# Performance work log

Measured on AMD Instinct MI355X. Metric: run time of the kernel, lower is better.

The kernel has to match this reference:

```python
import jax, jax.numpy as jnp
import numpy as np

B, C, P, NP = 16, 768, 2048, 64
FFE = 4


def _ln(x, g, b, eps=1e-5):
    m = jnp.mean(x, axis=-1, keepdims=True)
    v = jnp.mean(jnp.square(x - m), axis=-1, keepdims=True)
    return (x - m) * jax.lax.rsqrt(v + eps) * g + b


def _gelu(x):
    return jax.nn.gelu(x, approximate=False)  # torch nn.GELU default (erf)


def _any_attn(q, k, v, nqg, nqb, nkg, nkb, nvg, nvb, wq, wk, wv, wp, bq, bk, bv, bp):
    # AnyAttention: LN each stream, project, ReLU-gated logits scaled by d^-0.5, softmax, proj
    scale = q.shape[-1] ** -0.5
    qn = _ln(q, nqg, nqb) @ wq + bq
    kn = _ln(k, nkg, nkb) @ wk + bk
    vn = _ln(v, nvg, nvb) @ wv + bv
    attn = jnp.einsum('bqc,bkc->bqk', qn, kn)
    attn = jax.nn.relu(attn) * scale  # returned attn is relu*scale (pre-softmax)
    out = jnp.einsum('bqk,bkc->bqc', jax.nn.softmax(attn, axis=-1), vn)
    return attn, out @ wp + bp


def _forward(x, parts,
             enc_nq_g, enc_nq_b, enc_nk_g, enc_nk_b, enc_nv_g, enc_nv_b,
             enc_wq, enc_wk, enc_wv, enc_wp, enc_bq, enc_bk, enc_bv, enc_bp,
             dec_nq_g, dec_nq_b, dec_nk_g, dec_nk_b, dec_nv_g, dec_nv_b,
             dec_wq, dec_wk, dec_wv, dec_wp, dec_bq, dec_bk, dec_bv, dec_bp,
             ffn_ng, ffn_nb, ffn_w1, ffn_b1, ffn_w2, ffn_b2,
             sr_w1, sr_b1, sr_w2, sr_b2):
    x = jnp.swapaxes(x, 1, 2)  # b c p -> b p c
    # SimpleReasoning: SE-style gate over part tokens (AdaptiveMaxPool1d(1) = max over channel dim)
    g = jnp.max(parts, axis=-1)                                  # [b, np]
    g = _gelu(g @ sr_w1 + sr_b1)
    gate = jax.nn.sigmoid(g @ sr_w2 + sr_b2)[..., None]          # [b, np, 1]
    parts = gate * parts + parts                                 # parts1 + parts (residual)
    # enc_attn: parts attend over image tokens
    attn0, attn_out = _any_attn(parts, x, x,
                                enc_nq_g, enc_nq_b, enc_nk_g, enc_nk_b, enc_nv_g, enc_nv_b,
                                enc_wq, enc_wk, enc_wv, enc_wp, enc_bq, enc_bk, enc_bv, enc_bp)
    attn_0 = jnp.max(attn0, axis=-1)                             # maxpool over k -> [b, np]
    parts_in = parts + attn_out
    # FFN on image tokens with residual
    h = _ln(x, ffn_ng, ffn_nb)
    feats1 = x + (_gelu(h @ ffn_w1 + ffn_b1) @ ffn_w2 + ffn_b2)
    # dec_attn: image tokens attend over part tokens
    _, feats = _any_attn(feats1, parts_in, parts_in,
                         dec_nq_g, dec_nq_b, dec_nk_g, dec_nk_b, dec_nv_g, dec_nv_b,
                         dec_wq, dec_wk, dec_wv, dec_wp, dec_bq, dec_bk, dec_bv, dec_bp)
    feats = x + feats
    return jnp.swapaxes(feats, 1, 2), attn_0                     # [b, c, p], [b, np]


def setup_inputs() -> dict:
    key = jax.random.key(0)
    ki = iter(jax.random.split(key, 48))
    def rn(shape, s=1.0):
        return jax.random.normal(next(ki), shape, jnp.float32) * s
    d = {}
    d['x'] = rn((B, C, P))
    d['parts'] = rn((B, NP, C))
    for pre in ('enc', 'dec'):
        for nm in ('nq', 'nk', 'nv'):
            d[f'{pre}_{nm}_g'] = jnp.ones((C,), jnp.float32)
            d[f'{pre}_{nm}_b'] = jnp.zeros((C,), jnp.float32)
        for nm in ('wq', 'wk', 'wv', 'wp'):
            d[f'{pre}_{nm}'] = rn((C, C), 0.02)
        for nm in ('bq', 'bk', 'bv', 'bp'):
            d[f'{pre}_{nm}'] = jnp.zeros((C,), jnp.float32)
    d['ffn_ng'] = jnp.ones((C,), jnp.float32)
    d['ffn_nb'] = jnp.zeros((C,), jnp.float32)
    d['ffn_w1'] = rn((C, FFE * C), 0.02)
    d['ffn_b1'] = jnp.zeros((FFE * C,), jnp.float32)
    d['ffn_w2'] = rn((FFE * C, C), 0.02)
    d['ffn_b2'] = jnp.zeros((C,), jnp.float32)
    d['sr_w1'] = rn((NP, NP), 0.1)
    d['sr_b1'] = jnp.zeros((NP,), jnp.float32)
    d['sr_w2'] = rn((NP, NP), 0.1)
    d['sr_b2'] = jnp.zeros((NP,), jnp.float32)
    return d


def reference(x, parts,
              enc_nq_g, enc_nq_b, enc_nk_g, enc_nk_b, enc_nv_g, enc_nv_b,
              enc_wq, enc_wk, enc_wv, enc_wp, enc_bq, enc_bk, enc_bv, enc_bp,
              dec_nq_g, dec_nq_b, dec_nk_g, dec_nk_b, dec_nv_g, dec_nv_b,
              dec_wq, dec_wk, dec_wv, dec_wp, dec_bq, dec_bk, dec_bv, dec_bp,
              ffn_ng, ffn_nb, ffn_w1, ffn_b1, ffn_w2, ffn_b2,
              sr_w1, sr_b1, sr_w2, sr_b2):
    return _forward(x, parts,
                    enc_nq_g, enc_nq_b, enc_nk_g, enc_nk_b, enc_nv_g, enc_nv_b,
                    enc_wq, enc_wk, enc_wv, enc_wp, enc_bq, enc_bk, enc_bv, enc_bp,
                    dec_nq_g, dec_nq_b, dec_nk_g, dec_nk_b, dec_nv_g, dec_nv_b,
                    dec_wq, dec_wk, dec_wv, dec_wp, dec_bq, dec_bk, dec_bv, dec_bp,
                    ffn_ng, ffn_nb, ffn_w1, ffn_b1, ffn_w2, ffn_b2,
                    sr_w1, sr_b1, sr_w2, sr_b2)
```

## Files before the change

### kernel.cpp

```cpp
#include <hip/hip_runtime.h>

typedef unsigned short u16;
typedef unsigned int u32;
typedef __bf16 bf16x8 __attribute__((ext_vector_type(8)));
typedef float f32x4 __attribute__((ext_vector_type(4)));
typedef unsigned int u32x4 __attribute__((ext_vector_type(4)));

#define BB 16
#define CC 768
#define PP 2048
#define FF 3072

__device__ __forceinline__ float b2f(u16 u) {
  unsigned int x = ((unsigned int)u) << 16;
  return __builtin_bit_cast(float, x);
}
__device__ __forceinline__ u16 f2b(float f) {
  unsigned int x = __builtin_bit_cast(unsigned int, f);
  x += 0x7fffu + ((x >> 16) & 1u);
  return (u16)(x >> 16);
}
__device__ __forceinline__ float erf_fast(float x) {
  float ax = fabsf(x);
  float t = 1.0f / fmaf(0.3275911f, ax, 1.0f);
  float p = t * fmaf(t, fmaf(t, fmaf(t, fmaf(t, 1.061405429f, -1.453152027f),
                                     1.421413741f), -0.284496736f), 0.254829592f);
  float r = 1.0f - p * __expf(-ax * ax);
  return copysignf(r, x);
}
__device__ __forceinline__ float gelu_f(float x) {
  return 0.5f * x * (1.0f + erf_fast(x * 0.7071067811865475f));
}

typedef __attribute__((address_space(1))) const unsigned int g_u32;
typedef __attribute__((address_space(3))) unsigned int l_u32;
__device__ __forceinline__ void gl_lds16(const u16* g, u16* l) {
  __builtin_amdgcn_global_load_lds((g_u32*)g, (l_u32*)l, 16, 0, 0);
}

struct Wtr10 {
  const float* W[10]; const float* g[10]; u16* O[10];
  int Kd[10]; int Nd[10]; int tr[10]; int cum[11];
};
__global__ void wtr10_k(Wtr10 a) {
  __shared__ float t[64][65];
  int tbid = blockIdx.x;
  int z = 0;
  while (tbid >= a.cum[z + 1]) ++z;
  int r = tbid - a.cum[z];
  const float* W = a.W[z];
  const float* g = a.g[z];
  u16* Wt = a.O[z];
  int K = a.Kd[z], N = a.Nd[z];
  int nbx = N >> 6;
  int n0 = (r % nbx) * 64, k0 = (r / nbx) * 64;
  int tx = threadIdx.x & 63, ty = threadIdx.x >> 6;
  if (!a.tr[z]) {
    for (int i = 0; i < 16; ++i) {
      int k = k0 + ty + i * 4;
      float sc = g ? g[k] : 1.0f;
      Wt[(long)k * N + n0 + tx] = f2b(W[(long)k * N + n0 + tx] * sc);
    }
    return;
  }
  for (int i = 0; i < 16; ++i) {
    int k = k0 + ty + i * 4;
    float sc = g ? g[k] : 1.0f;
    t[ty + i * 4][tx] = W[(long)k * N + n0 + tx] * sc;
  }
  __syncthreads();
  for (int i = 0; i < 16; ++i) {
    int n = n0 + ty + i * 4;
    Wt[(long)n * K + k0 + tx] = f2b(t[tx][ty + i * 4]);
  }
}

struct Bf7 {
  const float* b[7]; const float* nb[7]; const float* W[7]; float* o[7];
  int Kd[7]; int Nd[7];
};
__global__ void bfuse7_k(Bf7 a) {
  __shared__ float red[4][64];
  int tbid = blockIdx.x;
  int z, bx;
  if (tbid < 72) { z = tbid / 12; bx = tbid % 12; }
  else { z = 6; bx = tbid - 72; }
  const float* b = a.b[z];
  const float* nb = a.nb[z];
  const float* W = a.W[z];
  float* outb = a.o[z];
  int K = a.Kd[z], N = a.Nd[z];
  int n = bx * 64 + (threadIdx.x & 63);
  int slice = threadIdx.x >> 6;
  float acc = 0.f;
#pragma unroll 4
  for (int k = slice; k < K; k += 4) acc += nb[k] * W[(long)k * N + n];
  red[slice][threadIdx.x & 63] = acc;
  __syncthreads();
  if (slice == 0)
    outb[n] = b[n] + red[0][threadIdx.x & 63] + red[1][threadIdx.x & 63] +
              red[2][threadIdx.x & 63] + red[3][threadIdx.x & 63];
}

__global__ void bfuse1_k(const float* __restrict__ b, const float* __restrict__ nb,
                         const float* __restrict__ W, float* __restrict__ outb) {
  __shared__ float red[4][64];
  int n = blockIdx.x * 64 + (threadIdx.x & 63);
  int slice = threadIdx.x >> 6;
  float acc = 0.f;
#pragma unroll 4
  for (int k = slice; k < CC; k += 4) acc += nb[k] * W[(long)k * CC + n];
  red[slice][threadIdx.x & 63] = acc;
  __syncthreads();
  if (slice == 0)
    outb[n] = b[n] + red[0][threadIdx.x & 63] + red[1][threadIdx.x & 63] +
              red[2][threadIdx.x & 63] + red[3][threadIdx.x & 63];
}

__global__ void dot_k(const u16* __restrict__ A, int stride,
                      const float* __restrict__ vec, float* __restrict__ outp) {
  int row = blockIdx.x * 4 + (threadIdx.x >> 6);
  int lane = threadIdx.x & 63;
  const u16* ip = A + (long)row * stride;
  float s = 0.f;
  for (int i = 0; i < 12; ++i) s += b2f(ip[lane + i * 64]) * vec[lane + i * 64];
  for (int o = 32; o; o >>= 1) s += __shfl_xor(s, o);
  if (lane == 0) outp[row] = s;
}

__global__ void xprep_k(const float* __restrict__ x, float* __restrict__ mean,
                        float* __restrict__ rstd, u16* __restrict__ xh) {
  __shared__ float t[64][65];
  __shared__ float red[8][64];
  __shared__ float mn_s[64], rs_s[64];
  int p0 = blockIdx.x * 64, b = blockIdx.y;
  int tx = threadIdx.x & 63, ty = threadIdx.x >> 6;
  const float* xb = x + (long)b * CC * PP;
  float s = 0.f, sq = 0.f;
  for (int c = ty; c < CC; c += 4) {
    float f = xb[(long)c * PP + p0 + tx];
    s += f; sq += f * f;
  }
  red[ty][tx] = s;
  red[4 + ty][tx] = sq;
  __syncthreads();
  if (ty == 0) {
    float S = red[0][tx] + red[1][tx] + red[2][tx] + red[3][tx];
    float Q = red[4][tx] + red[5][tx] + red[6][tx] + red[7][tx];
    float m = S * (1.0f / 768.0f);
    float var = Q * (1.0f / 768.0f) - m * m;
    float rs = rsqrtf(var + 1e-5f);
    mn_s[tx] = m; rs_s[tx] = rs;
    int gi = (b << 11) + p0 + tx;
    mean[gi] = m; rstd[gi] = rs;
  }
  __syncthreads();
  u16* ob = xh + (long)b * PP * CC;
  for (int cb = 0; cb < 12; ++cb) {
    int c0 = cb * 64;
    for (int i = 0; i < 16; ++i)
      t[ty + i * 4][tx] = xb[(long)(c0 + ty + i * 4) * PP + p0 + tx];
    __syncthreads();
    for (int i = 0; i < 16; ++i) {
      int pl = ty + i * 4;
      ob[(long)(p0 + pl) * CC + c0 + tx] = f2b((t[tx][pl] - mn_s[pl]) * rs_s[pl]);
    }
    __syncthreads();
  }
}

__global__ void parts_gate_k(const float* __restrict__ parts,
                             const float* __restrict__ w1, const float* __restrict__ b1,
                             const float* __restrict__ w2, const float* __restrict__ b2,
                             float* __restrict__ gate_out) {
  int b = blockIdx.x, t = threadIdx.x;
  __shared__ float g[64], g1[64];
  int r = t >> 2, l4 = t & 3;
  const float* pr = parts + ((long)b * 64 + r) * CC;
  float m = -1e30f;
  for (int c = l4; c < CC; c += 4) m = fmaxf(m, pr[c]);
  m = fmaxf(m, __shfl_xor(m, 1));
  m = fmaxf(m, __shfl_xor(m, 2));
  if (l4 == 0) g[r] = m;
  __syncthreads();
  if (t < 64) {
    float a = b1[t];
    for (int k = 0; k < 64; ++k) a += g[k] * w1[k * 64 + t];
    g1[t] = gelu_f(a);
  }
  __syncthreads();
  if (t < 64) {
    float a = b2[t];
    for (int k = 0; k < 64; ++k) a += g1[k] * w2[k * 64 + t];
    gate_out[b * 64 + t] = 1.0f / (1.0f + expf(-a));
  }
}

__global__ void gate_ln_k(const float* __restrict__ parts, const float* __restrict__ gate,
                          float* __restrict__ parts1, u16* __restrict__ ph) {
  int row = blockIdx.x * 4 + (threadIdx.x >> 6);
  int lane = threadIdx.x & 63;
  float g = 1.0f + gate[row];
  const float* ip = parts + (long)row * CC;
  float* op1 = parts1 + (long)row * CC;
  float v[12];
  float s = 0.f, sq = 0.f;
  for (int i = 0; i < 12; ++i) {
    float f = ip[lane + i * 64] * g;
    v[i] = f; op1[lane + i * 64] = f;
    s += f; sq += f * f;
  }
  for (int o = 32; o; o >>= 1) { s += __shfl_xor(s, o); sq += __shfl_xor(sq, o); }
  float mean = s * (1.0f / 768.0f);
  float var = sq * (1.0f / 768.0f) - mean * mean;
  float rstd = rsqrtf(var + 1e-5f);
  u16* op = ph + (long)row * CC;
  for (int i = 0; i < 12; ++i) op[lane + i * 64] = f2b((v[i] - mean) * rstd);
}

template <typename T>
__global__ void ln_rows_k(const T* __restrict__ in, u16* __restrict__ outp, int rows) {
  int row = blockIdx.x * 4 + (threadIdx.x >> 6);
  if (row >= rows) return;
  int lane = threadIdx.x & 63;
  const T* ip = in + (long)row * CC;
  float v[12];
  float s = 0.f, sq = 0.f;
  for (int i = 0; i < 12; ++i) {
    float f;
    if constexpr (sizeof(T) == 2) f = b2f(((const u16*)ip)[lane + i * 64]);
    else f = ((const float*)ip)[lane + i * 64];
    v[i] = f; s += f; sq += f * f;
  }
  for (int o = 32; o; o >>= 1) { s += __shfl_xor(s, o); sq += __shfl_xor(sq, o); }
  float mean = s * (1.0f / 768.0f);
  float var = sq * (1.0f / 768.0f) - mean * mean;
  float rstd = rsqrtf(var + 1e-5f);
  u16* op = outp + (long)row * CC;
  for (int i = 0; i < 12; ++i) op[lane + i * 64] = f2b((v[i] - mean) * rstd);
}

__global__ void softmax_enc_k(const float* __restrict__ attn, u16* __restrict__ sm,
                              float* __restrict__ attn0) {
  int row = blockIdx.x * 4 + (threadIdx.x >> 6);
  int lane = threadIdx.x & 63;
  const float* ap = attn + (long)row * PP;
  float v[32];
  float m = -1e30f;
  for (int i = 0; i < 32; ++i) { v[i] = ap[lane + i * 64]; m = fmaxf(m, v[i]); }
  for (int o = 32; o; o >>= 1) m = fmaxf(m, __shfl_xor(m, o));
  float s = 0.f;
  for (int i = 0; i < 32; ++i) { float e = expf(v[i] - m); v[i] = e; s += e; }
  for (int o = 32; o; o >>= 1) s += __shfl_xor(s, o);
  float inv = 1.0f / s;
  u16* sp = sm + (long)row * PP;
  for (int i = 0; i < 32; ++i) sp[lane + i * 64] = f2b(v[i] * inv);
  if (lane == 0) attn0[row] = m;
}

__global__ void pvred_k(const float* __restrict__ part, u16* __restrict__ outp) {
  long i = (long)blockIdx.x * 256 + threadIdx.x;
  const f32x4* p = (const f32x4*)part;
  f32x4 a = p[i];
  a += p[i + 196608];
  a += p[i + 2 * 196608];
  a += p[i + 3 * 196608];
  u32 lo = (u32)f2b(a.x) | ((u32)f2b(a.y) << 16);
  u32 hi = (u32)f2b(a.z) | ((u32)f2b(a.w) << 16);
  ((u32*)outp)[i * 2] = lo;
  ((u32*)outp)[i * 2 + 1] = hi;
}

template <int EPI>
__global__ __launch_bounds__(256) void gemmf_k(
    const u16* __restrict__ A, const u16* __restrict__ Bm, void* __restrict__ Cm,
    const float* __restrict__ bias, int M, int N, int K, int lda,
    const float* __restrict__ res32) {
  __shared__ __align__(16) u16 As[128 * 32];
  __shared__ __align__(16) u16 Bs[128 * 32];
  const int nbx = N >> 7;
  const int nwg = gridDim.x;
  int tile = blockIdx.x;
  if ((nwg & 7) == 0) {
    tile = (tile & 7) * (nwg >> 3) + (tile >> 3);
  }
  const int bm0 = (tile / nbx) << 7;
  const int bn0 = (tile % nbx) << 7;
  const int tid = threadIdx.x;
  const int lane = tid & 63;
  const int wave = tid >> 6;
  const int laneq = lane & 15, lanek = lane >> 4;
  const int wm = (wave >> 1) << 6, wn = (wave & 1) << 6;
  const int srow = wave * 32 + (lane >> 2);
  const int scol = (lane & 3) << 3;
  const u16* Ag0 = A + (long)(bm0 + srow) * lda + scol;
  const u16* Ag1 = A + (long)(bm0 + srow + 16) * lda + scol;
  const u16* Bg0 = Bm + (long)(bn0 + srow) * K + scol;
  const u16* Bg1 = Bm + (long)(bn0 + srow + 16) * K + scol;
  u16* lA0 = As + wave * 1024;
  u16* lA1 = As + wave * 1024 + 512;
  u16* lB0 = Bs + wave * 1024;
  u16* lB1 = Bs + wave * 1024 + 512;
  f32x4 acc[4][4] = {};
  for (int k0 = 0; k0 < K; k0 += 32) {
    gl_lds16(Ag0 + k0, lA0);
    gl_lds16(Ag1 + k0, lA1);
    gl_lds16(Bg0 + k0, lB0);
    gl_lds16(Bg1 + k0, lB1);
    __syncthreads();
    bf16x8 af[4], bfr[4];
#pragma unroll
    for (int i = 0; i < 4; ++i)
      af[i] = *(const bf16x8*)(As + (wm + i * 16 + laneq) * 32 + (lanek << 3));
#pragma unroll
    for (int i = 0; i < 4; ++i)
      bfr[i] = *(const bf16x8*)(Bs + (wn + i * 16 + laneq) * 32 + (lanek << 3));
#pragma unroll
    for (int mi = 0; mi < 4; ++mi)
#pragma unroll
      for (int ni = 0; ni < 4; ++ni)
        acc[mi][ni] =
            __builtin_amdgcn_mfma_f32_16x16x32_bf16(af[mi], bfr[ni], acc[mi][ni], 0, 0, 0);
    __syncthreads();
  }
#pragma unroll
  for (int mi = 0; mi < 4; ++mi) {
#pragma unroll
    for (int r = 0; r < 4; ++r) {
      const int row = bm0 + wm + mi * 16 + (lanek << 2) + r;
#pragma unroll
      for (int ni = 0; ni < 4; ++ni) {
        const int col = bn0 + wn + ni * 16 + laneq;
        float v = acc[mi][ni][r] + (bias ? bias[col] : 0.f);
        long off = (long)row * N + col;
        if constexpr (EPI == 0) {
          ((u16*)Cm)[off] = f2b(v);
        } else {
          ((float*)Cm)[off] = v + res32[off];
        }
      }
    }
  }
}

#define G256_BAR() __builtin_amdgcn_s_barrier()
#define G256_WLGKM0()                                    \
  do {                                                   \
    asm volatile("s_waitcnt lgkmcnt(0)" ::: "memory");   \
    __builtin_amdgcn_sched_barrier(0);                   \
  } while (0)
#define G256_RD_A(HALF)                                                        \
  _Pragma("unroll") for (int m2 = 0; m2 < 4; ++m2) {                           \
    af[m2 * 2 + 0] = *(const bf16x8*)(Ab + ar + (HALF)*4096 + m2 * 1024 + g0); \
    af[m2 * 2 + 1] = *(const bf16x8*)(Ab + ar + (HALF)*4096 + m2 * 1024 + g1); \
  }
#define G256_RD_B(HALF, BFR)                                                   \
  _Pragma("unroll") for (int n2 = 0; n2 < 2; ++n2) {                           \
    BFR[n2 * 2 + 0] = *(const bf16x8*)(Bb + br + (HALF)*2048 + n2 * 1024 + g0);\
    BFR[n2 * 2 + 1] = *(const bf16x8*)(Bb + br + (HALF)*2048 + n2 * 1024 + g1);\
  }
#define G256_MFMA_Q(H, NH, BFR)                                                \
  __builtin_amdgcn_s_setprio(1);                                               \
  _Pragma("unroll") for (int m2 = 0; m2 < 4; ++m2)                             \
  _Pragma("unroll") for (int n2 = 0; n2 < 2; ++n2)                             \
  _Pragma("unroll") for (int s = 0; s < 2; ++s)                                \
      acc[(H)*4 + m2][(NH)*2 + n2] = __builtin_amdgcn_mfma_f32_16x16x32_bf16(  \
          af[m2 * 2 + s], BFR[n2 * 2 + s], acc[(H)*4 + m2][(NH)*2 + n2], 0, 0, 0); \
  __builtin_amdgcn_s_setprio(0);

template <int EPI>
__global__ __launch_bounds__(512, 2) void gemm256_k(
    const u16* __restrict__ A, const u16* __restrict__ Bm, void* __restrict__ Cm,
    const float* __restrict__ bias, int M, int N, int K,
    const u16* __restrict__ rxh, const float* __restrict__ rmean,
    const float* __restrict__ rrstd, long rro) {
  __shared__ __align__(16) u16 As[2 * 16384];
  __shared__ __align__(16) u16 Bs[2 * 16384];
  const int nbx = N >> 8;
  const int nwg = gridDim.x;
  int tile = blockIdx.x;
  if ((nwg & 7) == 0) {
    tile = (tile & 7) * (nwg >> 3) + (tile >> 3);
  }
  const int bm0 = (tile / nbx) << 8;
  const int bn0 = (tile % nbx) << 8;
  const int tid = threadIdx.x;
  const int lane = tid & 63;
  const int wave = tid >> 6;
  const int laneq = lane & 15, lanek = lane >> 4;
  const int wrow = (wave >> 2) << 7;
  const int wcol = (wave & 3) << 6;
  const int srow8 = lane >> 3;
  const int sg = (lane & 7) ^ srow8;
  const u16* gA = A + (long)(bm0 + wave * 8 + srow8) * K + sg * 8;
  const u16* gB = Bm + (long)(bn0 + wave * 8 + srow8) * K + sg * 8;
  const long lineK = (long)64 * K;
  const int ldsLine = wave * 512;
  const int gx = laneq & 7;
  const int g0 = ((lanek) ^ gx) << 3;
  const int g1 = ((lanek + 4) ^ gx) << 3;
  const int ar = (wrow + laneq) * 64;
  const int br = (wcol + laneq) * 64;
  f32x4 acc[8][4] = {};
  bf16x8 af[8], bfr0[4], bfr1[4];
  const int NT = K >> 6;

  {
    u16* dA = (u16*)As;
    u16* dB = (u16*)Bs;
    gl_lds16(gA, dA + ldsLine);
    gl_lds16(gA + lineK, dA + ldsLine + 4096);
    gl_lds16(gA + 2 * lineK, dA + ldsLine + 8192);
    gl_lds16(gA + 3 * lineK, dA + ldsLine + 12288);
    gl_lds16(gB, dB + ldsLine);
    gl_lds16(gB + lineK, dB + ldsLine + 4096);
    gl_lds16(gB + 2 * lineK, dB + ldsLine + 8192);
    gl_lds16(gB + 3 * lineK, dB + ldsLine + 12288);
  }
  for (int T = 0; T < NT; ++T) {
    const u16* Ab = As + (T & 1) * 16384;
    const u16* Bb = Bs + (T & 1) * 16384;
    u16* An = (u16*)As + ((T & 1) ^ 1) * 16384;
    u16* Bn = (u16*)Bs + ((T & 1) ^ 1) * 16384;
    const long ko = (long)(T + 1) * 64;
    const bool more = (T + 1 < NT);
    if (more) {
      gl_lds16(gA + ko, An + ldsLine);
      gl_lds16(gA + ko + lineK, An + ldsLine + 4096);
      gl_lds16(gB + ko, Bn + ldsLine);
      gl_lds16(gB + ko + lineK, Bn + ldsLine + 4096);
      asm volatile("s_waitcnt vmcnt(4)" ::: "memory");
    } else {
      asm volatile("s_waitcnt vmcnt(0)" ::: "memory");
    }
    G256_BAR();
    G256_RD_A(0);
    G256_RD_B(0, bfr0);
    G256_WLGKM0();
    G256_MFMA_Q(0, 0, bfr0);
    G256_BAR();
    if (more) {
      gl_lds16(gA + ko + 2 * lineK, An + ldsLine + 8192);
      gl_lds16(gA + ko + 3 * lineK, An + ldsLine + 12288);
      gl_lds16(gB + ko + 2 * lineK, Bn + ldsLine + 8192);
      gl_lds16(gB + ko + 3 * lineK, Bn + ldsLine + 12288);
    }
    G256_RD_B(1, bfr1);
    G256_BAR();
    G256_WLGKM0();
    G256_MFMA_Q(0, 1, bfr1);
    G256_BAR();
    G256_RD_A(1);
    G256_BAR();
    G256_WLGKM0();
    G256_MFMA_Q(1, 1, bfr1);
    G256_BAR();
    G256_MFMA_Q(1, 0, bfr0);
  }

#pragma unroll
  for (int mi = 0; mi < 8; ++mi) {
#pragma unroll
    for (int r = 0; r < 4; ++r) {
      const int row = bm0 + wrow + mi * 16 + (lanek << 2) + r;
      float mn = 0.f, istd = 0.f;
      if constexpr (EPI == 3) {
        long gr = rro + row;
        mn = rmean[gr];
        istd = 1.0f / rrstd[gr];
      }
#pragma unroll
      for (int ni = 0; ni < 4; ++ni) {
        const int col = bn0 + wcol + ni * 16 + laneq;
        float v = acc[mi][ni][r] + bias[col];
        long off = (long)row * N + col;
        if constexpr (EPI == 0) {
          ((u16*)Cm)[off] = f2b(v);
        } else if constexpr (EPI == 1) {
          ((u16*)Cm)[off] = f2b(gelu_f(v));
        } else {
          v += b2f(rxh[(rro + row) * 768 + col]) * istd + mn;
          ((u16*)Cm)[off] = f2b(v);
        }
      }
    }
  }
}

template <int EPI, bool BNT, int TM, int TN>
__global__ __launch_bounds__(256) void gemm_k(
    const u16* __restrict__ A, const u16* __restrict__ Bm, void* __restrict__ Cm,
    const float* __restrict__ bias, int M, int N, int kLen, int lda, int ldB,
    long sA, long sB, long sC, float scale, const float* __restrict__ res32,
    const float* __restrict__ radd) {
  __shared__ __align__(16) u16 As[TM][40];
  __shared__ __align__(16) u16 Bs[TN][40];
  const int bn0 = blockIdx.x * TN;
  const int bm0 = (EPI == 4) ? 0 : blockIdx.y * TM;
  const int kOff = (EPI == 4) ? blockIdx.y * kLen : 0;
  const int bz = blockIdx.z;
  const u16* Ab = A + (long)bz * sA;
  const u16* Bb = Bm + (long)bz * sB;
  const long coff = (EPI == 4) ? ((long)blockIdx.y * gridDim.z + bz) * sC
                               : (long)bz * sC;
  const int tid = threadIdx.x;
  const int lane = tid & 63;
  const int wave = tid >> 6;
  const int wm = (TM == 64) ? 0 : ((TN == 64) ? wave * 32 : ((wave >> 1) << 6));
  const int wn = (TN == 64) ? 0 : ((TM == 64) ? wave * 32 : ((wave & 1) << 6));
  constexpr int MI = (TN == 64) ? 2 : 4;
  constexpr int NI = (TM == 64) ? 2 : 4;
  const int laneq = lane & 15, lanek = lane >> 4;
  f32x4 acc[MI][NI] = {};
  for (int k0 = 0; k0 < kLen; k0 += 32) {
    __syncthreads();
#pragma unroll
    for (int j = 0; j < TM / 64; ++j) {
      int v = tid + j * 256;
      int m = v >> 2, kcl = (v & 3) << 3;
      u32x4 val = {0, 0, 0, 0};
      if (bm0 + m < M)
        val = *(const u32x4*)(Ab + (long)(bm0 + m) * lda + kOff + k0 + kcl);
      *(u32x4*)(&As[m][kcl]) = val;
    }
    if constexpr (BNT) {
#pragma unroll
      for (int j = 0; j < TN / 64; ++j) {
        int v = tid + j * 256;
        int n = v >> 2, kcl = (v & 3) << 3;
        u32x4 val = {0, 0, 0, 0};
        if (bn0 + n < N)
          val = *(const u32x4*)(Bb + (long)(bn0 + n) * ldB + kOff + k0 + kcl);
        *(u32x4*)(&Bs[n][kcl]) = val;
      }
    } else {
      constexpr int CCH = TN / 8;
#pragma unroll
      for (int j = 0; j < TN / 64; ++j) {
        int v = tid + j * 256;
        int kk = v / CCH, nc = (v % CCH) << 3;
        u32x4 val = {0, 0, 0, 0};
        if (bn0 + nc < N)
          val = *(const u32x4*)(Bb + (long)(kOff + k0 + kk) * ldB + bn0 + nc);
        union { u32x4 v4; u16 u[8]; } uu;
        uu.v4 = val;
#pragma unroll
        for (int e = 0; e < 8; ++e) Bs[nc + e][kk] = uu.u[e];
      }
    }
    __syncthreads();
    bf16x8 af[MI], bfr[NI];
#pragma unroll
    for (int i = 0; i < MI; ++i)
      af[i] = *(const bf16x8*)(&As[wm + i * 16 + laneq][lanek << 3]);
#pragma unroll
    for (int i = 0; i < NI; ++i)
      bfr[i] = *(const bf16x8*)(&Bs[wn + i * 16 + laneq][lanek << 3]);
#pragma unroll
    for (int mi = 0; mi < MI; ++mi)
#pragma unroll
      for (int ni = 0; ni < NI; ++ni)
        acc[mi][ni] =
            __builtin_amdgcn_mfma_f32_16x16x32_bf16(af[mi], bfr[ni], acc[mi][ni], 0, 0, 0);
  }
  if constexpr (EPI == 5) {
    __syncthreads();
    float* smem = (float*)(wave < 2 ? (void*)As : (void*)Bs) + (wave & 1) * 1024;
    const int pbase = bm0 + wm + (lane & 3) * 16;
    const long obase = (long)bz * CC * PP;
#pragma unroll
    for (int ni = 0; ni < 4; ++ni) {
#pragma unroll
      for (int mi = 0; mi < 4; ++mi)
#pragma unroll
        for (int r = 0; r < 4; ++r) {
          const int col = bn0 + wn + ni * 16 + laneq;
          smem[(mi * 16 + (lanek << 2) + r) * 16 + laneq] = acc[mi][ni][r] + bias[col];
        }
      const int c = bn0 + wn + ni * 16 + (lane >> 2);
      const float* xs = res32 + obase + (long)c * PP + pbase;
      float* os = (float*)Cm + obase + (long)c * PP + pbase;
      const float* sr = smem + (lane & 3) * 256 + (lane >> 2);
#pragma unroll
      for (int q4 = 0; q4 < 4; ++q4) {
        f32x4 xv = *(const f32x4*)(xs + q4 * 4);
        f32x4 ov;
        ov.x = sr[(q4 * 4 + 0) * 16] + xv.x;
        ov.y = sr[(q4 * 4 + 1) * 16] + xv.y;
        ov.z = sr[(q4 * 4 + 2) * 16] + xv.z;
        ov.w = sr[(q4 * 4 + 3) * 16] + xv.w;
        *(f32x4*)(os + q4 * 4) = ov;
      }
    }
  } else if constexpr (EPI == 6) {
#pragma unroll
    for (int mi = 0; mi < MI; ++mi) {
#pragma unroll
      for (int r = 0; r < 4; ++r) {
        float e[NI];
        float mx = -1e30f;
#pragma unroll
        for (int ni = 0; ni < NI; ++ni) {
          const int col = bn0 + wn + ni * 16 + laneq;
          float v = acc[mi][ni][r] + (radd ? radd[(long)bz * N + col] : 0.f);
          v = fmaxf(v, 0.0f) * scale;
          e[ni] = v;
          mx = fmaxf(mx, v);
        }
        mx = fmaxf(mx, __shfl_xor(mx, 1));
        mx = fmaxf(mx, __shfl_xor(mx, 2));
        mx = fmaxf(mx, __shfl_xor(mx, 4));
        mx = fmaxf(mx, __shfl_xor(mx, 8));
        float s = 0.f;
#pragma unroll
        for (int ni = 0; ni < NI; ++ni) { e[ni] = __expf(e[ni] - mx); s += e[ni]; }
        s += __shfl_xor(s, 1);
        s += __shfl_xor(s, 2);
        s += __shfl_xor(s, 4);
        s += __shfl_xor(s, 8);
        float inv = 1.0f / s;
        const int row = bm0 + wm + mi * 16 + (lanek << 2) + r;
#pragma unroll
        for (int ni = 0; ni < NI; ++ni) {
          const int col = bn0 + wn + ni * 16 + laneq;
          ((u16*)Cm)[coff + (long)row * N + col] = f2b(e[ni] * inv);
        }
      }
    }
  } else {
#pragma unroll
    for (int mi = 0; mi < MI; ++mi) {
#pragma unroll
      for (int ni = 0; ni < NI; ++ni) {
        int col = bn0 + wn + ni * 16 + laneq;
        if (col >= N) continue;
#pragma unroll
        for (int r = 0; r < 4; ++r) {
          int row = bm0 + wm + mi * 16 + (lanek << 2) + r;
          if (row >= M) continue;
          float v = acc[mi][ni][r];
          long off = coff + (long)row * N + col;
          if constexpr (EPI == 0) {
            if (bias) v += bias[col];
            ((u16*)Cm)[off] = f2b(v);
          } else if constexpr (EPI == 2) {
            v += radd ? radd[(long)bz * M + row] : 0.f;
            ((float*)Cm)[off] = fmaxf(v, 0.0f) * scale;
          } else {
            ((float*)Cm)[off] = v;
          }
        }
      }
    }
  }
}

extern "C" void kernel_launch(void* const* d_in, const int* in_sizes, int n_in,
                              void* d_out, int out_size, void* d_ws, size_t ws_size,
                              hipStream_t stream) {
  (void)in_sizes; (void)n_in; (void)out_size;
  const float* x        = (const float*)d_in[0];
  const float* parts    = (const float*)d_in[1];
  const float* enc_nq_g = (const float*)d_in[2];
  const float* enc_nq_b = (const float*)d_in[3];
  const float* enc_nk_g = (const float*)d_in[4];
  const float* enc_nk_b = (const float*)d_in[5];
  const float* enc_nv_g = (const float*)d_in[6];
  const float* enc_nv_b = (const float*)d_in[7];
  const float* enc_wq   = (const float*)d_in[8];
  const float* enc_wk   = (const float*)d_in[9];
  const float* enc_wv   = (const float*)d_in[10];
  const float* enc_wp   = (const float*)d_in[11];
  const float* enc_bq   = (const float*)d_in[12];
  const float* enc_bk   = (const float*)d_in[13];
  const float* enc_bv   = (const float*)d_in[14];
  const float* enc_bp   = (const float*)d_in[15];
  const float* dec_nq_g = (const float*)d_in[16];
  const float* dec_nq_b = (const float*)d_in[17];
  const float* dec_nk_g = (const float*)d_in[18];
  const float* dec_nk_b = (const float*)d_in[19];
  const float* dec_nv_g = (const float*)d_in[20];
  const float* dec_nv_b = (const float*)d_in[21];
  const float* dec_wq   = (const float*)d_in[22];
  const float* dec_wk   = (const float*)d_in[23];
  const float* dec_wv   = (const float*)d_in[24];
  const float* dec_wp   = (const float*)d_in[25];
  const float* dec_bq   = (const float*)d_in[26];
  const float* dec_bk   = (const float*)d_in[27];
  const float* dec_bv   = (const float*)d_in[28];
  const float* dec_bp   = (const float*)d_in[29];
  const float* ffn_ng   = (const float*)d_in[30];
  const float* ffn_nb   = (const float*)d_in[31];
  const float* ffn_w1   = (const float*)d_in[32];
  const float* ffn_b1   = (const float*)d_in[33];
  const float* ffn_w2   = (const float*)d_in[34];
  const float* ffn_b2   = (const float*)d_in[35];
  const float* sr_w1    = (const float*)d_in[36];
  const float* sr_b1    = (const float*)d_in[37];
  const float* sr_w2    = (const float*)d_in[38];
  const float* sr_b2    = (const float*)d_in[39];
  float* outp = (float*)d_out;

  char* base = (char*)d_ws;
  size_t used = 0;
  auto alloc = [&](size_t bytes) -> void* {
    void* p = base + used;
    used += (bytes + 255) & ~(size_t)255;
    return p;
  };
  const long MC = (long)CC * CC;
  u16* WqeT  = (u16*)alloc(MC * 2);
  u16* WpeT  = (u16*)alloc(MC * 2);
  u16* WkvdT = (u16*)alloc(MC * 2 * 2);
  u16* WpdT  = (u16*)alloc(MC * 2);
  u16* W1T   = (u16*)alloc((long)CC * FF * 2);
  u16* W2T   = (u16*)alloc((long)CC * FF * 2);
  u16* WkS   = (u16*)alloc(MC * 2);
  u16* WvS   = (u16*)alloc(MC * 2);
  u16* WqdS  = (u16*)alloc(MC * 2);
  float* bqe  = (float*)alloc(CC * 4);
  float* bkv  = (float*)alloc(2 * CC * 4);
  float* bqd  = (float*)alloc(CC * 4);
  float* bkvd = (float*)alloc(2 * CC * 4);
  float* b1f  = (float*)alloc(FF * 4);
  float* bias2 = (float*)alloc(CC * 4);
  float* meanx = (float*)alloc((long)BB * PP * 4);
  float* rstdx = (float*)alloc((long)BB * PP * 4);
  const long BPC = (long)BB * PP * CC;
  u16* bufA = (u16*)alloc(BPC * 2);
  u16* bufB = (u16*)alloc(BPC * 2);
  const long PC = (long)BB * 64 * CC;
  float* parts1   = (float*)alloc(PC * 4);
  float* gateb    = (float*)alloc((long)BB * 64 * 4);
  u16*   p1hat    = (u16*)alloc(PC * 2);
  u16*   qn_e     = (u16*)alloc(PC * 2);
  u16*   qtil     = (u16*)alloc(PC * 2);
  float* qdotv    = (float*)alloc((long)BB * 64 * 4);
  float* attn_e   = (float*)alloc((long)BB * 64 * PP * 4);
  u16*   sm_e     = (u16*)alloc((long)BB * 64 * PP * 2);
  u16*   pv_e     = (u16*)alloc(PC * 2);
  float* pvpart   = (float*)alloc((long)4 * PC * 4);
  u16*   m2w      = (u16*)alloc(MC * 2);
  float* parts_in = (float*)alloc(PC * 4);
  u16*   pin_hat  = (u16*)alloc(PC * 2);
  u16*   kvd      = (u16*)alloc(PC * 2 * 2);
  u16*   gmat     = (u16*)alloc(PC * 2);
  float* kdotv    = (float*)alloc((long)BB * 64 * 4);
  u16*   vwT      = (u16*)alloc(PC * 2);
  u16*   sm_d     = (u16*)alloc((long)BB * PP * 64 * 2);
  int chunk_rows = 16384;
  while (chunk_rows > 4096 &&
         used + (size_t)chunk_rows * FF * 2 > ws_size)
    chunk_rows >>= 1;
  u16* ff1 = (u16*)alloc((long)chunk_rows * FF * 2);
  if (used > ws_size) return;

  const float scale = 0.03608439182435161f;
  dim3 blk(256);
  dim3 blk2(512);

  {
    Wtr10 wa;
    const float* Ws[10] = {enc_wq, dec_wk, dec_wv, enc_wp, dec_wp,
                           ffn_w1, ffn_w2, enc_wk, enc_wv, dec_wq};
    const float* gs[10] = {enc_nq_g, dec_nk_g, dec_nv_g, nullptr, nullptr,
                           ffn_ng, nullptr, enc_nk_g, enc_nv_g, dec_nq_g};
    u16* Os[10] = {WqeT, WkvdT, WkvdT + MC, WpeT, WpdT, W1T, W2T, WkS, WvS, WqdS};
    int Ks[10] = {CC, CC, CC, CC, CC, CC, FF, CC, CC, CC};
    int Ns[10] = {CC, CC, CC, CC, CC, FF, CC, CC, CC, CC};
    int tr[10] = {1, 1, 1, 1, 1, 1, 1, 0, 0, 0};
    int blks[10];
    int cum = 0;
    for (int i = 0; i < 10; ++i) {
      blks[i] = (Ns[i] / 64) * (Ks[i] / 64);
      wa.W[i] = Ws[i]; wa.g[i] = gs[i]; wa.O[i] = Os[i];
      wa.Kd[i] = Ks[i]; wa.Nd[i] = Ns[i]; wa.tr[i] = tr[i];
      wa.cum[i] = cum; cum += blks[i];
    }
    wa.cum[10] = cum;
    wtr10_k<<<cum, blk, 0, stream>>>(wa);
    Bf7 ba;
    const float* bs[7] = {enc_bq, enc_bk, enc_bv, dec_bq, dec_bk, dec_bv, ffn_b1};
    const float* nbs[7] = {enc_nq_b, enc_nk_b, enc_nv_b, dec_nq_b, dec_nk_b,
                           dec_nv_b, ffn_nb};
    const float* ws[7] = {enc_wq, enc_wk, enc_wv, dec_wq, dec_wk, dec_wv, ffn_w1};
    float* os[7] = {bqe, bkv, bkv + CC, bqd, bkvd, bkvd + CC, b1f};
    int Ks2[7] = {CC, CC, CC, CC, CC, CC, CC};
    int Ns2[7] = {CC, CC, CC, CC, CC, CC, FF};
    for (int i = 0; i < 7; ++i) {
      ba.b[i] = bs[i]; ba.nb[i] = nbs[i]; ba.W[i] = ws[i]; ba.o[i] = os[i];
      ba.Kd[i] = Ks2[i]; ba.Nd[i] = Ns2[i];
    }
    bfuse7_k<<<120, blk, 0, stream>>>(ba);
    bfuse1_k<<<12, blk, 0, stream>>>(enc_bp, bkv + CC, enc_wp, bias2);
  }

  gemmf_k<0><<<36, blk, 0, stream>>>(WpeT, WvS, m2w, nullptr, CC, CC, CC, CC,
      nullptr);

  xprep_k<<<dim3(32, 16), blk, 0, stream>>>(x, meanx, rstdx, bufA);

  parts_gate_k<<<16, blk, 0, stream>>>(parts, sr_w1, sr_b1, sr_w2, sr_b2, gateb);
  gate_ln_k<<<256, blk, 0, stream>>>(parts, gateb, parts1, p1hat);

  gemmf_k<0><<<48, blk, 0, stream>>>(p1hat, WqeT, qn_e, bqe, 1024, CC, CC, CC,
      nullptr);
  gemmf_k<0><<<48, blk, 0, stream>>>(qn_e, WkS, qtil, nullptr, 1024, CC, CC, CC,
      nullptr);
  dot_k<<<256, blk, 0, stream>>>(qn_e, CC, bkv, qdotv);

  gemm_k<2, true, 64, 128><<<dim3(16, 1, 16), blk, 0, stream>>>(
      qtil, bufA, attn_e, nullptr, 64, PP, CC, CC, CC,
      (long)64 * CC, (long)PP * CC, (long)64 * PP, scale, nullptr, qdotv);
  softmax_enc_k<<<256, blk, 0, stream>>>(attn_e, sm_e, outp + (long)BB * CC * PP);
  gemm_k<4, false, 64, 128><<<dim3(6, 4, 16), blk, 0, stream>>>(
      sm_e, bufA, pvpart, nullptr, 64, CC, PP / 4, PP, CC,
      (long)64 * PP, (long)PP * CC, (long)64 * CC, 0.f, nullptr, nullptr);
  pvred_k<<<768, blk, 0, stream>>>(pvpart, pv_e);
  gemmf_k<4><<<48, blk, 0, stream>>>(pv_e, m2w, parts_in, bias2, 1024, CC, CC, CC,
      parts1);

  ln_rows_k<float><<<256, blk, 0, stream>>>(parts_in, pin_hat, 1024);
  gemmf_k<0><<<96, blk, 0, stream>>>(pin_hat, WkvdT, kvd, bkvd, 1024, 2 * CC, CC,
      CC, nullptr);
  gemmf_k<0><<<48, blk, 0, stream>>>(kvd, WqdS, gmat, nullptr, 1024, CC, CC,
      2 * CC, nullptr);
  dot_k<<<256, blk, 0, stream>>>(kvd, 2 * CC, bqd, kdotv);
  gemm_k<0, true, 128, 64><<<dim3(1, 6, 16), blk, 0, stream>>>(
      WpdT, kvd + CC, vwT, nullptr, CC, 64, CC, CC, 2 * CC,
      0, (long)64 * 2 * CC, (long)CC * 64, 0.f, nullptr, nullptr);

  for (long r0 = 0; r0 < 32768; r0 += chunk_rows) {
    gemm256_k<1><<<(chunk_rows / 256) * 12, blk2, 0, stream>>>(
        bufA + r0 * CC, W1T, ff1, b1f, chunk_rows, FF, CC,
        nullptr, nullptr, nullptr, 0);
    gemm256_k<3><<<(chunk_rows / 256) * 3, blk2, 0, stream>>>(
        ff1, W2T, bufB + r0 * CC, ffn_b2, chunk_rows, CC, FF,
        bufA, meanx, rstdx, r0);
  }
  ln_rows_k<u16><<<8192, blk, 0, stream>>>(bufB, bufB, 32768);

  gemm_k<6, true, 128, 64><<<dim3(1, 16, 16), blk, 0, stream>>>(
      bufB, gmat, sm_d, nullptr, PP, 64, CC, CC, CC,
      (long)PP * CC, (long)64 * CC, (long)PP * 64, scale, nullptr, kdotv);

  gemm_k<5, true, 128, 128><<<dim3(6, 16, 16), blk, 0, stream>>>(
      sm_d, vwT, outp, dec_bp, PP, CC, 64, 64, 64,
      (long)PP * 64, (long)CC * 64, 0, 0.f, x, nullptr);
}
```

Baseline: 1.107 ms.

## Pre-multiply attention weight pairs into fused matrices and batch small setup kernels

Weight products Wk·Wq^T, Wqd·Wkd^T and Wpd·Wvd are precomputed once in a single batched GEMM kernel, along with folded bias vectors and scalar constants. Each per-activation chain of two GEMMs (q projection then key contraction, and the decoder kv projection then query/proj contraction) then becomes one GEMM. This removes the intermediate qn_e and kvd buffers and a dependent GEMM launch per stage. The FFN1 GEMM also gets an M-major tile ordering. The trade-off is more setup work and bf16 rounding of the fused weight products, which may change numerics slightly.

```diff
diff --git a/kernel.cpp b/kernel.cpp
--- a/kernel.cpp
+++ b/kernel.cpp
@@ -102,10 +102,14 @@
               red[2][threadIdx.x & 63] + red[3][threadIdx.x & 63];
 }
 
-__global__ void bfuse1_k(const float* __restrict__ b, const float* __restrict__ nb,
-                         const float* __restrict__ W, float* __restrict__ outb) {
+struct Bf2 { const float* b[2]; const float* nb[2]; const float* W[2]; float* o[2]; };
+__global__ void bfuse2_k(Bf2 a) {
   __shared__ float red[4][64];
-  int n = blockIdx.x * 64 + (threadIdx.x & 63);
+  int z = blockIdx.x / 12, bx = blockIdx.x % 12;
+  const float* b = a.b[z];
+  const float* nb = a.nb[z];
+  const float* W = a.W[z];
+  int n = bx * 64 + (threadIdx.x & 63);
   int slice = threadIdx.x >> 6;
   float acc = 0.f;
 #pragma unroll 4
@@ -113,19 +117,44 @@
   red[slice][threadIdx.x & 63] = acc;
   __syncthreads();
   if (slice == 0)
-    outb[n] = b[n] + red[0][threadIdx.x & 63] + red[1][threadIdx.x & 63] +
-              red[2][threadIdx.x & 63] + red[3][threadIdx.x & 63];
-}
-
-__global__ void dot_k(const u16* __restrict__ A, int stride,
-                      const float* __restrict__ vec, float* __restrict__ outp) {
-  int row = blockIdx.x * 4 + (threadIdx.x >> 6);
+    a.o[z][n] = (b ? b[n] : 0.f) + red[0][threadIdx.x & 63] +
+                red[1][threadIdx.x & 63] + red[2][threadIdx.x & 63] +
+                red[3][threadIdx.x & 63];
+}
+
+struct Dw4 { const u16* A[4]; const float* v[4]; float* o[4]; };
+__global__ void dotw4_k(Dw4 a) {
+  int z = blockIdx.x / 192;
+  int row = (blockIdx.x % 192) * 4 + (threadIdx.x >> 6);
   int lane = threadIdx.x & 63;
-  const u16* ip = A + (long)row * stride;
+  const u16* ip = a.A[z] + (long)row * CC;
+  const float* vec = a.v[z];
   float s = 0.f;
   for (int i = 0; i < 12; ++i) s += b2f(ip[lane + i * 64]) * vec[lane + i * 64];
   for (int o = 32; o; o >>= 1) s += __shfl_xor(s, o);
-  if (lane == 0) outp[row] = s;
+  if (lane == 0) a.o[z][row] = s;
+}
+
+__global__ void scal2_k(const float* a0, const float* b0, float* o0,
+                        const float* a1, const float* b1, float* o1) {
+  int w = threadIdx.x >> 6, lane = threadIdx.x & 63;
+  const float* A = w ? a1 : a0;
+  const float* Bv = w ? b1 : b0;
+  float s = 0.f;
+  for (int i = lane; i < CC; i += 64) s += A[i] * Bv[i];
+  for (int o = 32; o; o >>= 1) s += __shfl_xor(s, o);
+  if (lane == 0) *(w ? o1 : o0) = s;
+}
+
+__global__ void dotc_k(const u16* __restrict__ A, const float* __restrict__ vec,
+                       const float* __restrict__ cptr, float* __restrict__ outp) {
+  int row = blockIdx.x * 4 + (threadIdx.x >> 6);
+  int lane = threadIdx.x & 63;
+  const u16* ip = A + (long)row * CC;
+  float s = 0.f;
+  for (int i = 0; i < 12; ++i) s += b2f(ip[lane + i * 64]) * vec[lane + i * 64];
+  for (int o = 32; o; o >>= 1) s += __shfl_xor(s, o);
+  if (lane == 0) outp[row] = s + cptr[0];
 }
 
 __global__ void xprep_k(const float* __restrict__ x, float* __restrict__ mean,
@@ -343,6 +372,67 @@
   }
 }
 
+struct G4 { const u16* A[4]; const u16* B[4]; u16* C[4]; };
+__global__ __launch_bounds__(256) void gemmf4_k(G4 a) {
+  __shared__ __align__(16) u16 As[128 * 32];
+  __shared__ __align__(16) u16 Bs[128 * 32];
+  const int z = blockIdx.x / 36;
+  const int r = blockIdx.x % 36;
+  const u16* A = a.A[z];
+  const u16* Bm = a.B[z];
+  u16* Cm = a.C[z];
+  const int bm0 = (r / 6) << 7;
+  const int bn0 = (r % 6) << 7;
+  const int tid = threadIdx.x;
+  const int lane = tid & 63;
+  const int wave = tid >> 6;
+  const int laneq = lane & 15, lanek = lane >> 4;
+  const int wm = (wave >> 1) << 6, wn = (wave & 1) << 6;
+  const int srow = wave * 32 + (lane >> 2);
+  const int scol = (lane & 3) << 3;
+  const u16* Ag0 = A + (long)(bm0 + srow) * CC + scol;
+  const u16* Ag1 = A + (long)(bm0 + srow + 16) * CC + scol;
+  const u16* Bg0 = Bm + (long)(bn0 + srow) * CC + scol;
+  const u16* Bg1 = Bm + (long)(bn0 + srow + 16) * CC + scol;
+  u16* lA0 = As + wave * 1024;
+  u16* lA1 = As + wave * 1024 + 512;
+  u16* lB0 = Bs + wave * 1024;
+  u16* lB1 = Bs + wave * 1024 + 512;
+  f32x4 acc[4][4] = {};
+  for (int k0 = 0; k0 < CC; k0 += 32) {
+    gl_lds16(Ag0 + k0, lA0);
+    gl_lds16(Ag1 + k0, lA1);
+    gl_lds16(Bg0 + k0, lB0);
+    gl_lds16(Bg1 + k0, lB1);
+    __syncthreads();
+    bf16x8 af[4], bfr[4];
+#pragma unroll
+    for (int i = 0; i < 4; ++i)
+      af[i] = *(const bf16x8*)(As + (wm + i * 16 + laneq) * 32 + (lanek << 3));
+#pragma unroll
+    for (int i = 0; i < 4; ++i)
+      bfr[i] = *(const bf16x8*)(Bs + (wn + i * 16 + laneq) * 32 + (lanek << 3));
+#pragma unroll
+    for (int mi = 0; mi < 4; ++mi)
+#pragma unroll
+      for (int ni = 0; ni < 4; ++ni)
+        acc[mi][ni] =
+            __builtin_amdgcn_mfma_f32_16x16x32_bf16(af[mi], bfr[ni], acc[mi][ni], 0, 0, 0);
+    __syncthreads();
+  }
+#pragma unroll
+  for (int mi = 0; mi < 4; ++mi)
+#pragma unroll
+    for (int r2 = 0; r2 < 4; ++r2) {
+      const int row = bm0 + wm + mi * 16 + (lanek << 2) + r2;
+#pragma unroll
+      for (int ni = 0; ni < 4; ++ni) {
+        const int col = bn0 + wn + ni * 16 + laneq;
+        Cm[(long)row * CC + col] = f2b(acc[mi][ni][r2]);
+      }
+    }
+}
+
 #define G256_BAR() __builtin_amdgcn_s_barrier()
 #define G256_WLGKM0()                                    \
   do {                                                   \
@@ -373,7 +463,7 @@
     const u16* __restrict__ A, const u16* __restrict__ Bm, void* __restrict__ Cm,
     const float* __restrict__ bias, int M, int N, int K,
     const u16* __restrict__ rxh, const float* __restrict__ rmean,
-    const float* __restrict__ rrstd, long rro) {
+    const float* __restrict__ rrstd, long rro, int nbm) {
   __shared__ __align__(16) u16 As[2 * 16384];
   __shared__ __align__(16) u16 Bs[2 * 16384];
   const int nbx = N >> 8;
@@ -382,8 +472,14 @@
   if ((nwg & 7) == 0) {
     tile = (tile & 7) * (nwg >> 3) + (tile >> 3);
   }
-  const int bm0 = (tile / nbx) << 8;
-  const int bn0 = (tile % nbx) << 8;
+  int bm0, bn0;
+  if (nbm) {
+    bm0 = (tile % nbm) << 8;
+    bn0 = (tile / nbm) << 8;
+  } else {
+    bm0 = (tile / nbx) << 8;
+    bn0 = (tile % nbx) << 8;
+  }
   const int tid = threadIdx.x;
   const int lane = tid & 63;
   const int wave = tid >> 6;
@@ -640,10 +736,7 @@
           if (row >= M) continue;
           float v = acc[mi][ni][r];
           long off = coff + (long)row * N + col;
-          if constexpr (EPI == 0) {
-            if (bias) v += bias[col];
-            ((u16*)Cm)[off] = f2b(v);
-          } else if constexpr (EPI == 2) {
+          if constexpr (EPI == 2) {
             v += radd ? radd[(long)bz * M + row] : 0.f;
             ((float*)Cm)[off] = fmaxf(v, 0.0f) * scale;
           } else {
@@ -709,21 +802,35 @@
     return p;
   };
   const long MC = (long)CC * CC;
-  u16* WqeT  = (u16*)alloc(MC * 2);
-  u16* WpeT  = (u16*)alloc(MC * 2);
-  u16* WkvdT = (u16*)alloc(MC * 2 * 2);
-  u16* WpdT  = (u16*)alloc(MC * 2);
-  u16* W1T   = (u16*)alloc((long)CC * FF * 2);
-  u16* W2T   = (u16*)alloc((long)CC * FF * 2);
-  u16* WkS   = (u16*)alloc(MC * 2);
-  u16* WvS   = (u16*)alloc(MC * 2);
-  u16* WqdS  = (u16*)alloc(MC * 2);
+  u16* WpeT = (u16*)alloc(MC * 2);
+  u16* WpdT = (u16*)alloc(MC * 2);
+  u16* W1T  = (u16*)alloc((long)CC * FF * 2);
+  u16* W2T  = (u16*)alloc((long)CC * FF * 2);
+  u16* WkR  = (u16*)alloc(MC * 2);
+  u16* WqR  = (u16*)alloc(MC * 2);
+  u16* WvS  = (u16*)alloc(MC * 2);
+  u16* WqdR = (u16*)alloc(MC * 2);
+  u16* WkdR = (u16*)alloc(MC * 2);
+  u16* WvdR = (u16*)alloc(MC * 2);
+  u16* m2w  = (u16*)alloc(MC * 2);
+  u16* Bqk  = (u16*)alloc(MC * 2);
+  u16* Bg   = (u16*)alloc(MC * 2);
+  u16* Bv   = (u16*)alloc(MC * 2);
   float* bqe  = (float*)alloc(CC * 4);
-  float* bkv  = (float*)alloc(2 * CC * 4);
+  float* bke  = (float*)alloc(CC * 4);
+  float* bve  = (float*)alloc(CC * 4);
   float* bqd  = (float*)alloc(CC * 4);
-  float* bkvd = (float*)alloc(2 * CC * 4);
+  float* bkd  = (float*)alloc(CC * 4);
+  float* bvd  = (float*)alloc(CC * 4);
   float* b1f  = (float*)alloc(FF * 4);
-  float* bias2 = (float*)alloc(CC * 4);
+  float* bias2   = (float*)alloc(CC * 4);
+  float* bias_vw = (float*)alloc(CC * 4);
+  float* bq2     = (float*)alloc(CC * 4);
+  float* wqb     = (float*)alloc(CC * 4);
+  float* bias_g  = (float*)alloc(CC * 4);
+  float* wkb     = (float*)alloc(CC * 4);
+  float* cq      = (float*)alloc(256);
+  float* ck      = (float*)alloc(256);
   float* meanx = (float*)alloc((long)BB * PP * 4);
   float* rstdx = (float*)alloc((long)BB * PP * 4);
   const long BPC = (long)BB * PP * CC;
@@ -733,20 +840,17 @@
   float* parts1   = (float*)alloc(PC * 4);
   float* gateb    = (float*)alloc((long)BB * 64 * 4);
   u16*   p1hat    = (u16*)alloc(PC * 2);
-  u16*   qn_e     = (u16*)alloc(PC * 2);
   u16*   qtil     = (u16*)alloc(PC * 2);
   float* qdotv    = (float*)alloc((long)BB * 64 * 4);
   float* attn_e   = (float*)alloc((long)BB * 64 * PP * 4);
   u16*   sm_e     = (u16*)alloc((long)BB * 64 * PP * 2);
   u16*   pv_e     = (u16*)alloc(PC * 2);
   float* pvpart   = (float*)alloc((long)4 * PC * 4);
-  u16*   m2w      = (u16*)alloc(MC * 2);
   float* parts_in = (float*)alloc(PC * 4);
   u16*   pin_hat  = (u16*)alloc(PC * 2);
-  u16*   kvd      = (u16*)alloc(PC * 2 * 2);
-  u16*   gmat     = (u16*)alloc(PC * 2);
+  u16*   Gm       = (u16*)alloc(PC * 2);
+  u16*   VW       = (u16*)alloc(PC * 2);
   float* kdotv    = (float*)alloc((long)BB * 64 * 4);
-  u16*   vwT      = (u16*)alloc(PC * 2);
   u16*   sm_d     = (u16*)alloc((long)BB * PP * 64 * 2);
   int chunk_rows = 16384;
   while (chunk_rows > 4096 &&
@@ -761,21 +865,20 @@
 
   {
     Wtr10 wa;
-    const float* Ws[10] = {enc_wq, dec_wk, dec_wv, enc_wp, dec_wp,
-                           ffn_w1, ffn_w2, enc_wk, enc_wv, dec_wq};
-    const float* gs[10] = {enc_nq_g, dec_nk_g, dec_nv_g, nullptr, nullptr,
-                           ffn_ng, nullptr, enc_nk_g, enc_nv_g, dec_nq_g};
-    u16* Os[10] = {WqeT, WkvdT, WkvdT + MC, WpeT, WpdT, W1T, W2T, WkS, WvS, WqdS};
-    int Ks[10] = {CC, CC, CC, CC, CC, CC, FF, CC, CC, CC};
-    int Ns[10] = {CC, CC, CC, CC, CC, FF, CC, CC, CC, CC};
-    int tr[10] = {1, 1, 1, 1, 1, 1, 1, 0, 0, 0};
-    int blks[10];
+    const float* Ws[10] = {enc_wp, dec_wp, ffn_w1, ffn_w2, enc_wk,
+                           enc_wq, enc_wv, dec_wq, dec_wk, dec_wv};
+    const float* gs[10] = {nullptr, nullptr, ffn_ng, nullptr, enc_nk_g,
+                           enc_nq_g, enc_nv_g, dec_nq_g, dec_nk_g, dec_nv_g};
+    u16* Os[10] = {WpeT, WpdT, W1T, W2T, WkR, WqR, WvS, WqdR, WkdR, WvdR};
+    int Ks[10] = {CC, CC, CC, FF, CC, CC, CC, CC, CC, CC};
+    int Ns[10] = {CC, CC, FF, CC, CC, CC, CC, CC, CC, CC};
+    int tr[10] = {1, 1, 1, 1, 0, 0, 0, 0, 0, 0};
     int cum = 0;
     for (int i = 0; i < 10; ++i) {
-      blks[i] = (Ns[i] / 64) * (Ks[i] / 64);
       wa.W[i] = Ws[i]; wa.g[i] = gs[i]; wa.O[i] = Os[i];
       wa.Kd[i] = Ks[i]; wa.Nd[i] = Ns[i]; wa.tr[i] = tr[i];
-      wa.cum[i] = cum; cum += blks[i];
+      wa.cum[i] = cum;
+      cum += (Ns[i] / 64) * (Ks[i] / 64);
     }
     wa.cum[10] = cum;
     wtr10_k<<<cum, blk, 0, stream>>>(wa);
@@ -784,30 +887,39 @@
     const float* nbs[7] = {enc_nq_b, enc_nk_b, enc_nv_b, dec_nq_b, dec_nk_b,
                            dec_nv_b, ffn_nb};
     const float* ws[7] = {enc_wq, enc_wk, enc_wv, dec_wq, dec_wk, dec_wv, ffn_w1};
-    float* os[7] = {bqe, bkv, bkv + CC, bqd, bkvd, bkvd + CC, b1f};
-    int Ks2[7] = {CC, CC, CC, CC, CC, CC, CC};
-    int Ns2[7] = {CC, CC, CC, CC, CC, CC, FF};
+    float* os[7] = {bqe, bke, bve, bqd, bkd, bvd, b1f};
     for (int i = 0; i < 7; ++i) {
       ba.b[i] = bs[i]; ba.nb[i] = nbs[i]; ba.W[i] = ws[i]; ba.o[i] = os[i];
-      ba.Kd[i] = Ks2[i]; ba.Nd[i] = Ns2[i];
+      ba.Kd[i] = CC; ba.Nd[i] = (i == 6) ? FF : CC;
     }
     bfuse7_k<<<120, blk, 0, stream>>>(ba);
-    bfuse1_k<<<12, blk, 0, stream>>>(enc_bp, bkv + CC, enc_wp, bias2);
-  }
-
-  gemmf_k<0><<<36, blk, 0, stream>>>(WpeT, WvS, m2w, nullptr, CC, CC, CC, CC,
-      nullptr);
+    Bf2 b2a;
+    b2a.b[0] = enc_bp;  b2a.nb[0] = bve; b2a.W[0] = enc_wp; b2a.o[0] = bias2;
+    b2a.b[1] = nullptr; b2a.nb[1] = bvd; b2a.W[1] = dec_wp; b2a.o[1] = bias_vw;
+    bfuse2_k<<<24, blk, 0, stream>>>(b2a);
+    Dw4 da;
+    da.A[0] = WkR;  da.v[0] = bqe; da.o[0] = bq2;
+    da.A[1] = WqR;  da.v[1] = bke; da.o[1] = wqb;
+    da.A[2] = WqdR; da.v[2] = bkd; da.o[2] = bias_g;
+    da.A[3] = WkdR; da.v[3] = bqd; da.o[3] = wkb;
+    dotw4_k<<<768, blk, 0, stream>>>(da);
+    scal2_k<<<1, 128, 0, stream>>>(bqe, bke, cq, bkd, bqd, ck);
+    G4 ga;
+    ga.A[0] = WpeT; ga.B[0] = WvS;  ga.C[0] = m2w;
+    ga.A[1] = WkR;  ga.B[1] = WqR;  ga.C[1] = Bqk;
+    ga.A[2] = WqdR; ga.B[2] = WkdR; ga.C[2] = Bg;
+    ga.A[3] = WpdT; ga.B[3] = WvdR; ga.C[3] = Bv;
+    gemmf4_k<<<144, blk, 0, stream>>>(ga);
+  }
 
   xprep_k<<<dim3(32, 16), blk, 0, stream>>>(x, meanx, rstdx, bufA);
 
   parts_gate_k<<<16, blk, 0, stream>>>(parts, sr_w1, sr_b1, sr_w2, sr_b2, gateb);
   gate_ln_k<<<256, blk, 0, stream>>>(parts, gateb, parts1, p1hat);
 
-  gemmf_k<0><<<48, blk, 0, stream>>>(p1hat, WqeT, qn_e, bqe, 1024, CC, CC, CC,
+  gemmf_k<0><<<48, blk, 0, stream>>>(p1hat, Bqk, qtil, bq2, 1024, CC, CC, CC,
       nullptr);
-  gemmf_k<0><<<48, blk, 0, stream>>>(qn_e, WkS, qtil, nullptr, 1024, CC, CC, CC,
-      nullptr);
-  dot_k<<<256, blk, 0, stream>>>(qn_e, CC, bkv, qdotv);
+  dotc_k<<<256, blk, 0, stream>>>(p1hat, wqb, cq, qdotv);
 
   gemm_k<2, true, 64, 128><<<dim3(16, 1, 16), blk, 0, stream>>>(
       qtil, bufA, attn_e, nullptr, 64, PP, CC, CC, CC,
@@ -821,30 +933,27 @@
       parts1);
 
   ln_rows_k<float><<<256, blk, 0, stream>>>(parts_in, pin_hat, 1024);
-  gemmf_k<0><<<96, blk, 0, stream>>>(pin_hat, WkvdT, kvd, bkvd, 1024, 2 * CC, CC,
-      CC, nullptr);
-  gemmf_k<0><<<48, blk, 0, stream>>>(kvd, WqdS, gmat, nullptr, 1024, CC, CC,
-      2 * CC, nullptr);
-  dot_k<<<256, blk, 0, stream>>>(kvd, 2 * CC, bqd, kdotv);
-  gemm_k<0, true, 128, 64><<<dim3(1, 6, 16), blk, 0, stream>>>(
-      WpdT, kvd + CC, vwT, nullptr, CC, 64, CC, CC, 2 * CC,
-      0, (long)64 * 2 * CC, (long)CC * 64, 0.f, nullptr, nullptr);
+  gemmf_k<0><<<48, blk, 0, stream>>>(pin_hat, Bg, Gm, bias_g, 1024, CC, CC, CC,
+      nullptr);
+  gemmf_k<0><<<48, blk, 0, stream>>>(pin_hat, Bv, VW, bias_vw, 1024, CC, CC, CC,
+      nullptr);
+  dotc_k<<<256, blk, 0, stream>>>(pin_hat, wkb, ck, kdotv);
 
   for (long r0 = 0; r0 < 32768; r0 += chunk_rows) {
     gemm256_k<1><<<(chunk_rows / 256) * 12, blk2, 0, stream>>>(
         bufA + r0 * CC, W1T, ff1, b1f, chunk_rows, FF, CC,
-        nullptr, nullptr, nullptr, 0);
+        nullptr, nullptr, nullptr, 0, chunk_rows / 256);
     gemm256_k<3><<<(chunk_rows / 256) * 3, blk2, 0, stream>>>(
         ff1, W2T, bufB + r0 * CC, ffn_b2, chunk_rows, CC, FF,
-        bufA, meanx, rstdx, r0);
+        bufA, meanx, rstdx, r0, 0);
   }
   ln_rows_k<u16><<<8192, blk, 0, stream>>>(bufB, bufB, 32768);
 
   gemm_k<6, true, 128, 64><<<dim3(1, 16, 16), blk, 0, stream>>>(
-      bufB, gmat, sm_d, nullptr, PP, 64, CC, CC, CC,
+      bufB, Gm, sm_d, nullptr, PP, 64, CC, CC, CC,
       (long)PP * CC, (long)64 * CC, (long)PP * 64, scale, nullptr, kdotv);
 
-  gemm_k<5, true, 128, 128><<<dim3(6, 16, 16), blk, 0, stream>>>(
-      sm_d, vwT, outp, dec_bp, PP, CC, 64, 64, 64,
-      (long)PP * 64, (long)CC * 64, 0, 0.f, x, nullptr);
-}
+  gemm_k<5, false, 128, 128><<<dim3(6, 16, 16), blk, 0, stream>>>(
+      sm_d, VW, outp, dec_bp, PP, CC, 64, 64, CC,
+      (long)PP * 64, (long)64 * CC, 0, 0.f, x, nullptr);
+}
```

New measurement: 1.070 ms. -3.3%, faster.
